# Performance work log

Measured on AMD Instinct MI355X. Metric: run time of the kernel, lower is better.

Reference implementation:

```python
import jax, jax.numpy as jnp
import numpy as np
from math import sqrt

NUM_HEAD = 16
HEAD_DIM = 64  # out_dim // num_head = 1024 // 16


def setup_inputs() -> dict:
    key = jax.random.key(0)
    ks = jax.random.split(key, 6)
    B, L, D = 2, 2048, 1024
    s = 1.0 / sqrt(D)
    return {
        "x": jax.random.normal(ks[0], (B, L, D), jnp.float32),
        "position_embedding": jax.random.normal(ks[1], (1, NUM_HEAD, L, L), jnp.float32),
        "Wq": jax.random.normal(ks[2], (D, D), jnp.float32) * s,
        "Wk": jax.random.normal(ks[3], (D, D), jnp.float32) * s,
        "Wv": jax.random.normal(ks[4], (D, D), jnp.float32) * s,
        "Wo": jax.random.normal(ks[5], (D, D), jnp.float32) * s,
    }


def reference(x, position_embedding, Wq, Wk, Wv, Wo):
    # x: [B, L, D]; torch Linear(y = x @ W.T) -> here weights stored as [in, out]
    B, L, D = x.shape
    H, Hd = NUM_HEAD, HEAD_DIM
    q = (x @ Wq).reshape(B, L, H, Hd).transpose(0, 2, 1, 3)  # [B,H,L,Hd]
    k = (x @ Wk).reshape(B, L, H, Hd).transpose(0, 2, 1, 3)
    v = (x @ Wv).reshape(B, L, H, Hd).transpose(0, 2, 1, 3)
    scores = jnp.einsum("bhqd,bhkd->bhqk", q, k) / sqrt(Hd)  # [B,H,L,L]
    scores = scores + position_embedding
    attn = jax.nn.softmax(scores, axis=-1)
    out = jnp.einsum("bhqk,bhkd->bhqd", attn, v)  # [B,H,L,Hd]
    out = out.transpose(0, 2, 1, 3).reshape(B, L, H * Hd)
    return out @ Wo
```

## Files before the change

kernel.cpp:

```cpp
#include <hip/hip_runtime.h>
#include <hip/hip_bf16.h>
#include <stdint.h>

typedef __hip_bfloat16 bf16;
typedef __attribute__((ext_vector_type(8))) short bf16x8;
typedef __attribute__((ext_vector_type(4))) float f32x4;
typedef __attribute__((ext_vector_type(16))) float f32x16;
typedef __attribute__((ext_vector_type(4))) unsigned u32x4;

#define B_  2
#define L_  2048
#define D_  1024
#define H_  16
#define HD_ 64
#define BH_ 32
#define L2E 1.4426950408889634f

#define DEV static __device__ __forceinline__

DEV short f2bf(float f) {
    bf16 h = __float2bfloat16(f);
    return __builtin_bit_cast(short, h);
}

DEV unsigned pk2(float lo, float hi) {
    unsigned a = (unsigned short)__builtin_bit_cast(unsigned short, __float2bfloat16(lo));
    unsigned b = (unsigned short)__builtin_bit_cast(unsigned short, __float2bfloat16(hi));
    return a | (b << 16);
}

DEV f32x4 mfma16(bf16x8 a, bf16x8 b, f32x4 c) {
    return __builtin_amdgcn_mfma_f32_16x16x32_bf16(a, b, c, 0, 0, 0);
}
DEV f32x16 mfma32(bf16x8 a, bf16x8 b, f32x16 c) {
    return __builtin_amdgcn_mfma_f32_32x32x16_bf16(a, b, c, 0, 0, 0);
}

DEV void async_ld16(const void* g, void* lds_uniform) {
    __builtin_amdgcn_global_load_lds((const __attribute__((address_space(1))) void*)g,
                                     (__attribute__((address_space(3))) void*)lds_uniform,
                                     16, 0, 0);
}

DEV int swz(int row, int col) {
    int blk = (row << 3) + (col >> 3);
    blk ^= (row & 7);
    return (blk << 3) + (col & 7);
}

__global__ __launch_bounds__(256) void k_cast_x(const float* __restrict__ x,
                                                bf16* __restrict__ xb, int n8) {
    int i = blockIdx.x * 256 + threadIdx.x;
    if (i >= n8) return;
    const float4* src = (const float4*)x + (size_t)i * 2;
    float4 a = src[0], b = src[1];
    bf16x8 v;
    v[0]=f2bf(a.x); v[1]=f2bf(a.y); v[2]=f2bf(a.z); v[3]=f2bf(a.w);
    v[4]=f2bf(b.x); v[5]=f2bf(b.y); v[6]=f2bf(b.z); v[7]=f2bf(b.w);
    *(bf16x8*)(xb + (size_t)i * 8) = v;
}

__global__ __launch_bounds__(256) void k_cast_wT(const float* __restrict__ W0, const float* __restrict__ W1,
                                                 const float* __restrict__ W2, const float* __restrict__ W3,
                                                 bf16* __restrict__ WT) {
    const float* W = (blockIdx.z == 0) ? W0 : (blockIdx.z == 1) ? W1 : (blockIdx.z == 2) ? W2 : W3;
    __shared__ float tile[64][65];
    const int r0 = blockIdx.y * 64, c0 = blockIdx.x * 64;
    const int tx = threadIdx.x & 63, ty = threadIdx.x >> 6;
    #pragma unroll
    for (int i = 0; i < 16; ++i) {
        int r = ty + i * 4;
        tile[r][tx] = W[(size_t)(r0 + r) * D_ + c0 + tx];
    }
    __syncthreads();
    bf16* out = WT + (size_t)blockIdx.z * D_ * D_;
    #pragma unroll
    for (int i = 0; i < 16; ++i) {
        int n = ty + i * 4;
        out[(size_t)(c0 + n) * D_ + r0 + tx] = __float2bfloat16(tile[tx][n]);
    }
}

template <int MODE>
__global__ __launch_bounds__(256) void k_gemm(const bf16* __restrict__ A, const bf16* __restrict__ BT,
                                              void* __restrict__ C) {
    __shared__ __align__(16) bf16 As[128 * 64];
    __shared__ __align__(16) bf16 Bs[128 * 64];
    const int t = threadIdx.x;
    const int w = t >> 6, lane = t & 63;
    const int lr = lane & 15, lg = lane >> 4;
    const int wr = (w >> 1) * 64, wc = (w & 1) * 64;
    const size_t am0 = (size_t)blockIdx.y * 128;
    const size_t bn0 = (size_t)blockIdx.x * 128;

    f32x4 acc[4][4] = {};

    for (int kt = 0; kt < 1024 / 64; ++kt) {
        const int k0 = kt * 64;
        if (kt) __syncthreads();
        #pragma unroll
        for (int c = 0; c < 4; ++c) {
            int phys = c * 256 + t;
            int lb = phys ^ ((phys >> 3) & 7);
            int row = lb >> 3, cb = lb & 7;
            int ldsoff = (c * 256 + w * 64) * 8;
            async_ld16(A  + (am0 + row) * 1024 + k0 + cb * 8, (void*)(As + ldsoff));
            async_ld16(BT + (bn0 + row) * 1024 + k0 + cb * 8, (void*)(Bs + ldsoff));
        }
        __syncthreads();
        bf16x8 af[4][2], bfv[4][2];
        #pragma unroll
        for (int mi = 0; mi < 4; ++mi)
            #pragma unroll
            for (int ks = 0; ks < 2; ++ks)
                af[mi][ks] = *(const bf16x8*)(As + swz(wr + mi * 16 + lr, ks * 32 + lg * 8));
        #pragma unroll
        for (int ni = 0; ni < 4; ++ni)
            #pragma unroll
            for (int ks = 0; ks < 2; ++ks)
                bfv[ni][ks] = *(const bf16x8*)(Bs + swz(wc + ni * 16 + lr, ks * 32 + lg * 8));
        #pragma unroll
        for (int mi = 0; mi < 4; ++mi)
            #pragma unroll
            for (int ni = 0; ni < 4; ++ni) {
                acc[mi][ni] = mfma16(af[mi][0], bfv[ni][0], acc[mi][ni]);
                acc[mi][ni] = mfma16(af[mi][1], bfv[ni][1], acc[mi][ni]);
            }
    }

    #pragma unroll
    for (int mi = 0; mi < 4; ++mi)
        #pragma unroll
        for (int ni = 0; ni < 4; ++ni)
            #pragma unroll
            for (int j = 0; j < 4; ++j) {
                size_t gm = am0 + wr + mi * 16 + lg * 4 + j;
                size_t gn = bn0 + wc + ni * 16 + lr;
                float v = acc[mi][ni][j];
                if (MODE == 0) {
                    int which = (int)(gn >> 10);
                    int h = (int)((gn >> 6) & 15);
                    int d = (int)(gn & 63);
                    int bb = (int)(gm >> 11);
                    int l = (int)(gm & 2047);
                    if (which == 0) v *= 0.18033688011112042f;
                    bf16* dst = (bf16*)C + (size_t)which * ((size_t)BH_ * L_ * HD_);
                    dst[((size_t)(bb * H_ + h) * L_ + l) * HD_ + d] = __float2bfloat16(v);
                } else {
                    ((float*)C)[gm * 1024 + gn] = v;
                }
            }
}

__global__ __launch_bounds__(256) void k_transpose_v(const bf16* __restrict__ Vb, bf16* __restrict__ VTb) {
    __shared__ __align__(16) short tile[64][80];
    const int bh = blockIdx.y;
    const int l0 = blockIdx.x * 64;
    const int t = threadIdx.x;
    const int rr = t >> 2, cc = (t & 3) * 16;
    const short* src = (const short*)(Vb + ((size_t)bh * L_ + l0 + rr) * HD_ + cc);
    *(bf16x8*)&tile[rr][cc]     = *(const bf16x8*)src;
    *(bf16x8*)&tile[rr][cc + 8] = *(const bf16x8*)(src + 8);
    __syncthreads();
    bf16x8 v0, v1;
    #pragma unroll
    for (int i = 0; i < 8; ++i) v0[i] = tile[cc + i][rr];
    #pragma unroll
    for (int i = 0; i < 8; ++i) v1[i] = tile[cc + 8 + i][rr];
    short* dst = (short*)(VTb + ((size_t)bh * HD_ + rr) * L_ + l0 + cc);
    *(bf16x8*)dst       = v0;
    *(bf16x8*)(dst + 8) = v1;
}

__global__ __launch_bounds__(256, 3) void k_attn(const bf16* __restrict__ Qb, const bf16* __restrict__ Kb,
                                                 const bf16* __restrict__ VTb, const float* __restrict__ PE,
                                                 bf16* __restrict__ Ob) {
    __shared__ __align__(16) char shm[49152];

    const int bid = blockIdx.x;
    const int sw  = (bid & 7) * 64 + (bid >> 3);
    const int qt  = sw & 31, h = sw >> 5;
    const int t   = threadIdx.x;
    const int w   = t >> 6, l = t & 63;
    const int qs  = w & 1, b = w >> 1;
    const int q0  = qt * 64 + qs * 32;
    const int lq  = l & 31;
    const int lh  = l >> 5;

    const int pb = (lq >> 2) & 3;
    const int prow = lq + (pb == 1 ? 4 : (pb == 2 ? -4 : 0));

    bf16x8 Qf[4];
    #pragma unroll
    for (int dm = 0; dm < 4; ++dm)
        Qf[dm] = *(const bf16x8*)(Qb + ((size_t)(b * H_ + h) * L_ + q0 + lq) * HD_ + dm * 16 + lh * 8);

    const bf16*  kb  = Kb  + (size_t)(b * H_ + h) * L_ * HD_;
    const bf16*  vbp = VTb + (size_t)(b * H_ + h) * HD_ * L_;
    const float* peq = PE  + ((size_t)h * L_ + q0) * L_;

    const int k_srcoff  = (l >> 3) * HD_ + (((l & 7) ^ (l >> 3)) * 8);
    const int v_srcoff  = (l >> 2) * L_  + (((l & 3) ^ ((l >> 2) & 3)) * 8);
    const int pe_srcoff = (l >> 3) * L_  + (((l & 7) ^ (l >> 3)) * 4);

    int kro[4];
    #pragma unroll
    for (int dm = 0; dm < 4; ++dm)
        kro[dm] = prow * 64 + (((dm * 2 + lh) ^ (prow & 7)) * 8);
    int vro[2][2];
    #pragma unroll
    for (int d0 = 0; d0 < 2; ++d0)
        #pragma unroll
        for (int m = 0; m < 2; ++m)
            vro[d0][m] = (d0 * 32 + lq) * 32 + (((m * 2 + lh) ^ (lq & 3)) * 8);
    int peo[4];
    #pragma unroll
    for (int g = 0; g < 4; ++g)
        peo[g] = lq * 32 + ((((g >> 1) * 4 + (g & 1) + lh * 2) ^ (lq & 7)) * 4);

#define SH_K(BUF)  (shm + (BUF) * 24576 + b * 4096)
#define SH_V(BUF)  (shm + (BUF) * 24576 + 8192 + b * 4096)
#define SH_PE(BUF) (shm + (BUF) * 24576 + 16384 + qs * 4096)

    f32x16 o[2] = {};
    float mrun = -3e38f, lpart = 0.f;

#define STAGE(BUF, TILE) {                                                              \
    const int kv0_ = (TILE) * 32;                                                       \
    _Pragma("unroll") for (int i = 0; i < 2; ++i) {                                     \
        const int c = 2 * qs + i;                                                       \
        async_ld16(kb + (size_t)(kv0_ + c * 8) * HD_ + k_srcoff, (void*)(SH_K(BUF) + c * 1024)); \
    }                                                                                   \
    _Pragma("unroll") for (int i = 0; i < 2; ++i) {                                     \
        const int c = 2 * qs + i;                                                       \
        async_ld16(vbp + (size_t)(c * 16) * L_ + kv0_ + v_srcoff, (void*)(SH_V(BUF) + c * 1024)); \
    }                                                                                   \
    _Pragma("unroll") for (int i = 0; i < 2; ++i) {                                     \
        const int c = 2 * b + i;                                                        \
        async_ld16(peq + (size_t)(c * 8) * L_ + kv0_ + pe_srcoff, (void*)(SH_PE(BUF) + c * 1024)); \
    }                                                                                   \
}

#define COMPUTE(BUF) {                                                                  \
    const bf16*  KL = (const bf16*)SH_K(BUF);                                           \
    const bf16*  VL = (const bf16*)SH_V(BUF);                                           \
    const float* PL = (const float*)SH_PE(BUF);                                         \
    bf16x8 kf0_ = *(const bf16x8*)(KL + kro[0]);                                        \
    bf16x8 kf1_ = *(const bf16x8*)(KL + kro[1]);                                        \
    bf16x8 kf2_ = *(const bf16x8*)(KL + kro[2]);                                        \
    bf16x8 kf3_ = *(const bf16x8*)(KL + kro[3]);                                        \
    f32x16 s = {};                                                                      \
    s = mfma32(kf0_, Qf[0], s);                                                         \
    s = mfma32(kf1_, Qf[1], s);                                                         \
    s = mfma32(kf2_, Qf[2], s);                                                         \
    s = mfma32(kf3_, Qf[3], s);                                                         \
    float4 pef_[4];                                                                     \
    _Pragma("unroll") for (int g = 0; g < 4; ++g)                                       \
        pef_[g] = *(const float4*)(PL + peo[g]);                                        \
    float v_[16];                                                                       \
    _Pragma("unroll") for (int r = 0; r < 16; ++r)                                      \
        v_[r] = fmaf(pef_[r >> 2][r & 3], L2E, s[r]);                                   \
    float t0_ = fmaxf(fmaxf(v_[0], v_[1]), fmaxf(v_[2], v_[3]));                        \
    float t1_ = fmaxf(fmaxf(v_[4], v_[5]), fmaxf(v_[6], v_[7]));                        \
    float t2_ = fmaxf(fmaxf(v_[8], v_[9]), fmaxf(v_[10], v_[11]));                      \
    float t3_ = fmaxf(fmaxf(v_[12], v_[13]), fmaxf(v_[14], v_[15]));                    \
    float vmh_ = fmaxf(fmaxf(t0_, t1_), fmaxf(t2_, t3_));                               \
    float vm_ = fmaxf(vmh_, __shfl_xor(vmh_, 32, 64));                                  \
    float mold_ = mrun;                                                                 \
    float mnew_ = mold_;                                                                \
    if (!__all(vm_ <= mold_ + 10.f)) {                                                  \
        mnew_ = fmaxf(mold_, vm_);                                                      \
        float scl_ = __builtin_amdgcn_exp2f(mold_ - mnew_);                             \
        mrun = mnew_;                                                                   \
        lpart *= scl_;                                                                  \
        _Pragma("unroll") for (int r = 0; r < 16; ++r) { o[0][r] *= scl_; o[1][r] *= scl_; } \
    }                                                                                   \
    float p_[16], ssum_ = 0.f;                                                          \
    _Pragma("unroll") for (int r = 0; r < 16; ++r) {                                    \
        p_[r] = __builtin_amdgcn_exp2f(v_[r] - mnew_);                                  \
        ssum_ += p_[r];                                                                 \
    }                                                                                   \
    lpart += ssum_;                                                                     \
    unsigned a_[8];                                                                     \
    _Pragma("unroll") for (int j = 0; j < 8; ++j)                                       \
        a_[j] = pk2(p_[2 * j], p_[2 * j + 1]);                                          \
    u32x4 w0v_ = { a_[0], a_[1], a_[2], a_[3] };                                        \
    u32x4 w1v_ = { a_[4], a_[5], a_[6], a_[7] };                                        \
    bf16x8 pf0_ = __builtin_bit_cast(bf16x8, w0v_);                                     \
    bf16x8 pf1_ = __builtin_bit_cast(bf16x8, w1v_);                                     \
    o[0] = mfma32(*(const bf16x8*)(VL + vro[0][0]), pf0_, o[0]);                        \
    o[0] = mfma32(*(const bf16x8*)(VL + vro[0][1]), pf1_, o[0]);                        \
    o[1] = mfma32(*(const bf16x8*)(VL + vro[1][0]), pf0_, o[1]);                        \
    o[1] = mfma32(*(const bf16x8*)(VL + vro[1][1]), pf1_, o[1]);                        \
}

    STAGE(0, 0)
    STAGE(1, 1)
    asm volatile("s_waitcnt vmcnt(6)" ::: "memory");
    __builtin_amdgcn_s_barrier();

    for (int tt = 0; tt < 64; ++tt) {
        const int buf = tt & 1;
        if (buf == 0) { COMPUTE(0) } else { COMPUTE(1) }
        __builtin_amdgcn_s_barrier();
        const int pft = (tt + 2 < 64) ? tt + 2 : 63;
        if (buf == 0) { STAGE(0, pft) } else { STAGE(1, pft) }
        asm volatile("s_waitcnt vmcnt(6)" ::: "memory");
        __builtin_amdgcn_s_barrier();
    }
#undef COMPUTE
#undef STAGE
#undef SH_K
#undef SH_V
#undef SH_PE

    asm volatile("s_waitcnt vmcnt(0)" ::: "memory");

    float lsum = lpart + __shfl_xor(lpart, 32, 64);
    float inv = __builtin_amdgcn_rcpf(lsum);
    #pragma unroll
    for (int d0 = 0; d0 < 2; ++d0)
        #pragma unroll
        for (int r = 0; r < 16; r += 2) {
            float e0 = o[d0][r] * inv;
            float e1 = o[d0][r + 1] * inv;
            int d = d0 * 32 + ((r & 3) + 8 * (r >> 2)) + lh * 4;
            *(unsigned*)(Ob + ((size_t)b * L_ + q0 + lq) * D_ + h * HD_ + d) = pk2(e0, e1);
        }
}

extern "C" void kernel_launch(void* const* d_in, const int* in_sizes, int n_in,
                              void* d_out, int out_size, void* d_ws, size_t ws_size,
                              hipStream_t stream) {
    const float* x  = (const float*)d_in[0];
    const float* pe = (const float*)d_in[1];
    const float* Wq = (const float*)d_in[2];
    const float* Wk = (const float*)d_in[3];
    const float* Wv = (const float*)d_in[4];
    const float* Wo = (const float*)d_in[5];
    float* out = (float*)d_out;

    const size_t MD = (size_t)4096 * 1024;
    const size_t HS = (size_t)BH_ * L_ * HD_;

    bf16* Xb  = (bf16*)d_ws;
    bf16* WT  = Xb + MD;
    bf16* Qb  = WT + MD;
    bf16* Kb  = Qb + HS;
    bf16* Vb  = Kb + HS;
    bf16* VTb = Vb + HS;
    bf16* Ob  = VTb + HS;

    k_cast_x<<<2048, 256, 0, stream>>>(x, Xb, 4096 * 1024 / 8);
    k_cast_wT<<<dim3(16, 16, 4), 256, 0, stream>>>(Wq, Wk, Wv, Wo, WT);
    k_gemm<0><<<dim3(24, 32), 256, 0, stream>>>(Xb, WT, (void*)Qb);
    k_transpose_v<<<dim3(32, 32), 256, 0, stream>>>(Vb, VTb);
    k_attn<<<512, 256, 0, stream>>>(Qb, Kb, VTb, pe, Ob);
    k_gemm<1><<<dim3(8, 32), 256, 0, stream>>>(Ob, WT + (size_t)3072 * 1024, (void*)out);
}
```

Before: 172.9 us.

## Load position bias directly to registers and share V tile across batch waves

Position-embedding values are now loaded straight from global memory into registers, two tiles ahead, instead of being staged through LDS. V staging is rewritten so the four waves cooperatively load a shared 64-wide V tile covering both batches with a new swizzle, and the loop is unrolled by two so buffer indices are static. LDS use drops from 48KB to 32KB per block, which may allow more resident blocks, but PE register prefetch raises register pressure and the waitcnt accounting changes.

```diff
diff --git a/kernel.cpp b/kernel.cpp
--- a/kernel.cpp
+++ b/kernel.cpp
@@ -175,7 +175,7 @@
 __global__ __launch_bounds__(256, 3) void k_attn(const bf16* __restrict__ Qb, const bf16* __restrict__ Kb,
                                                  const bf16* __restrict__ VTb, const float* __restrict__ PE,
                                                  bf16* __restrict__ Ob) {
-    __shared__ __align__(16) char shm[49152];
+    __shared__ __align__(16) char shm[32768];
 
     const int bid = blockIdx.x;
     const int sw  = (bid & 7) * 64 + (bid >> 3);
@@ -195,13 +195,18 @@
     for (int dm = 0; dm < 4; ++dm)
         Qf[dm] = *(const bf16x8*)(Qb + ((size_t)(b * H_ + h) * L_ + q0 + lq) * HD_ + dm * 16 + lh * 8);
 
-    const bf16*  kb  = Kb  + (size_t)(b * H_ + h) * L_ * HD_;
-    const bf16*  vbp = VTb + (size_t)(b * H_ + h) * HD_ * L_;
-    const float* peq = PE  + ((size_t)h * L_ + q0) * L_;
-
-    const int k_srcoff  = (l >> 3) * HD_ + (((l & 7) ^ (l >> 3)) * 8);
-    const int v_srcoff  = (l >> 2) * L_  + (((l & 3) ^ ((l >> 2) & 3)) * 8);
-    const int pe_srcoff = (l >> 3) * L_  + (((l & 7) ^ (l >> 3)) * 4);
+    const bf16*  kb    = Kb  + (size_t)(b * H_ + h) * L_ * HD_;
+    const bf16*  vbase = VTb + (size_t)h * HD_ * L_;
+    const float* perow = PE  + ((size_t)h * L_ + q0 + lq) * L_;
+
+    const int k_srcoff = (l >> 3) * HD_ + (((l & 7) ^ (l >> 3)) * 8);
+    const int vlb   = (l & 7) ^ (l >> 3);
+    const size_t v_lane = (size_t)(vlb >> 2) * ((size_t)H_ * HD_ * L_)
+                        + (size_t)(l >> 3) * L_ + (vlb & 3) * 8;
+    int peoff[4];
+    #pragma unroll
+    for (int g = 0; g < 4; ++g)
+        peoff[g] = (g >> 1) * 16 + (g & 1) * 4 + lh * 8;
 
     int kro[4];
     #pragma unroll
@@ -212,18 +217,14 @@
     for (int d0 = 0; d0 < 2; ++d0)
         #pragma unroll
         for (int m = 0; m < 2; ++m)
-            vro[d0][m] = (d0 * 32 + lq) * 32 + (((m * 2 + lh) ^ (lq & 3)) * 8);
-    int peo[4];
-    #pragma unroll
-    for (int g = 0; g < 4; ++g)
-        peo[g] = lq * 32 + ((((g >> 1) * 4 + (g & 1) + lh * 2) ^ (lq & 7)) * 4);
-
-#define SH_K(BUF)  (shm + (BUF) * 24576 + b * 4096)
-#define SH_V(BUF)  (shm + (BUF) * 24576 + 8192 + b * 4096)
-#define SH_PE(BUF) (shm + (BUF) * 24576 + 16384 + qs * 4096)
+            vro[d0][m] = (d0 * 32 + lq) * 64 + (((b * 4 + m * 2 + lh) ^ (lq & 7)) * 8);
+
+#define SH_K(BUF) (shm + (BUF) * 16384 + b * 4096)
+#define SH_V(BUF) (shm + (BUF) * 16384 + 8192)
 
     f32x16 o[2] = {};
     float mrun = -3e38f, lpart = 0.f;
+    float4 pe0[4], pe1[4];
 
 #define STAGE(BUF, TILE) {                                                              \
     const int kv0_ = (TILE) * 32;                                                       \
@@ -232,19 +233,19 @@
         async_ld16(kb + (size_t)(kv0_ + c * 8) * HD_ + k_srcoff, (void*)(SH_K(BUF) + c * 1024)); \
     }                                                                                   \
     _Pragma("unroll") for (int i = 0; i < 2; ++i) {                                     \
-        const int c = 2 * qs + i;                                                       \
-        async_ld16(vbp + (size_t)(c * 16) * L_ + kv0_ + v_srcoff, (void*)(SH_V(BUF) + c * 1024)); \
+        const int cv = 2 * w + i;                                                       \
+        async_ld16(vbase + v_lane + (size_t)(cv * 8) * L_ + kv0_, (void*)(SH_V(BUF) + cv * 1024)); \
     }                                                                                   \
-    _Pragma("unroll") for (int i = 0; i < 2; ++i) {                                     \
-        const int c = 2 * b + i;                                                        \
-        async_ld16(peq + (size_t)(c * 8) * L_ + kv0_ + pe_srcoff, (void*)(SH_PE(BUF) + c * 1024)); \
-    }                                                                                   \
-}
-
-#define COMPUTE(BUF) {                                                                  \
-    const bf16*  KL = (const bf16*)SH_K(BUF);                                           \
-    const bf16*  VL = (const bf16*)SH_V(BUF);                                           \
-    const float* PL = (const float*)SH_PE(BUF);                                         \
+}
+
+#define PELOAD(DST, TILE) {                                                             \
+    _Pragma("unroll") for (int g = 0; g < 4; ++g)                                       \
+        DST[g] = *(const float4*)(perow + (size_t)(TILE) * 32 + peoff[g]);              \
+}
+
+#define COMPUTE(BUF, PEA) {                                                             \
+    const bf16* KL = (const bf16*)SH_K(BUF);                                            \
+    const bf16* VL = (const bf16*)SH_V(BUF);                                            \
     bf16x8 kf0_ = *(const bf16x8*)(KL + kro[0]);                                        \
     bf16x8 kf1_ = *(const bf16x8*)(KL + kro[1]);                                        \
     bf16x8 kf2_ = *(const bf16x8*)(KL + kro[2]);                                        \
@@ -254,12 +255,9 @@
     s = mfma32(kf1_, Qf[1], s);                                                         \
     s = mfma32(kf2_, Qf[2], s);                                                         \
     s = mfma32(kf3_, Qf[3], s);                                                         \
-    float4 pef_[4];                                                                     \
-    _Pragma("unroll") for (int g = 0; g < 4; ++g)                                       \
-        pef_[g] = *(const float4*)(PL + peo[g]);                                        \
     float v_[16];                                                                       \
     _Pragma("unroll") for (int r = 0; r < 16; ++r)                                      \
-        v_[r] = fmaf(pef_[r >> 2][r & 3], L2E, s[r]);                                   \
+        v_[r] = fmaf(PEA[r >> 2][r & 3], L2E, s[r]);                                    \
     float t0_ = fmaxf(fmaxf(v_[0], v_[1]), fmaxf(v_[2], v_[3]));                        \
     float t1_ = fmaxf(fmaxf(v_[4], v_[5]), fmaxf(v_[6], v_[7]));                        \
     float t2_ = fmaxf(fmaxf(v_[8], v_[9]), fmaxf(v_[10], v_[11]));                      \
@@ -295,24 +293,34 @@
 }
 
     STAGE(0, 0)
+    PELOAD(pe0, 0)
     STAGE(1, 1)
-    asm volatile("s_waitcnt vmcnt(6)" ::: "memory");
+    PELOAD(pe1, 1)
+    asm volatile("s_waitcnt vmcnt(8)" ::: "memory");
     __builtin_amdgcn_s_barrier();
 
-    for (int tt = 0; tt < 64; ++tt) {
-        const int buf = tt & 1;
-        if (buf == 0) { COMPUTE(0) } else { COMPUTE(1) }
+    for (int tp = 0; tp < 32; ++tp) {
+        const int e = 2 * tp;
+        const int pfA = (e + 2 < 64) ? e + 2 : 63;
+        const int pfB = (e + 3 < 64) ? e + 3 : 63;
+        COMPUTE(0, pe0)
         __builtin_amdgcn_s_barrier();
-        const int pft = (tt + 2 < 64) ? tt + 2 : 63;
-        if (buf == 0) { STAGE(0, pft) } else { STAGE(1, pft) }
-        asm volatile("s_waitcnt vmcnt(6)" ::: "memory");
+        STAGE(0, pfA)
+        PELOAD(pe0, pfA)
+        asm volatile("s_waitcnt vmcnt(8)" ::: "memory");
+        __builtin_amdgcn_s_barrier();
+        COMPUTE(1, pe1)
+        __builtin_amdgcn_s_barrier();
+        STAGE(1, pfB)
+        PELOAD(pe1, pfB)
+        asm volatile("s_waitcnt vmcnt(8)" ::: "memory");
         __builtin_amdgcn_s_barrier();
     }
 #undef COMPUTE
+#undef PELOAD
 #undef STAGE
 #undef SH_K
 #undef SH_V
-#undef SH_PE
 
     asm volatile("s_waitcnt vmcnt(0)" ::: "memory");
 
```

Measured after the change: 199.9 us. 15.6% more time.

## Triple-buffer attention K/V/PE staging and share V tile across batch warps

Applied to the files above, without the earlier changes.

Deepens the async global-to-LDS pipeline from two to three buffers, prefetching three tiles ahead with a wait that lets 12 loads stay in flight. The V tile layout is changed so that both batch halves are loaded into one shared 64-wide swizzled LDS region, with each warp loading a slice. LDS grows to 72KB, and launch bounds drop from 3 to 2 blocks per CU, trading occupancy for more latency hiding.

```diff
diff --git a/kernel.cpp b/kernel.cpp
--- a/kernel.cpp
+++ b/kernel.cpp
@@ -172,10 +172,10 @@
     *(bf16x8*)(dst + 8) = v1;
 }
 
-__global__ __launch_bounds__(256, 3) void k_attn(const bf16* __restrict__ Qb, const bf16* __restrict__ Kb,
+__global__ __launch_bounds__(256, 2) void k_attn(const bf16* __restrict__ Qb, const bf16* __restrict__ Kb,
                                                  const bf16* __restrict__ VTb, const float* __restrict__ PE,
                                                  bf16* __restrict__ Ob) {
-    __shared__ __align__(16) char shm[49152];
+    __shared__ __align__(16) char shm[73728];
 
     const int bid = blockIdx.x;
     const int sw  = (bid & 7) * 64 + (bid >> 3);
@@ -195,13 +195,15 @@
     for (int dm = 0; dm < 4; ++dm)
         Qf[dm] = *(const bf16x8*)(Qb + ((size_t)(b * H_ + h) * L_ + q0 + lq) * HD_ + dm * 16 + lh * 8);
 
-    const bf16*  kb  = Kb  + (size_t)(b * H_ + h) * L_ * HD_;
-    const bf16*  vbp = VTb + (size_t)(b * H_ + h) * HD_ * L_;
-    const float* peq = PE  + ((size_t)h * L_ + q0) * L_;
+    const bf16*  kb    = Kb  + (size_t)(b * H_ + h) * L_ * HD_;
+    const bf16*  vbase = VTb + (size_t)h * HD_ * L_;
+    const float* peq   = PE  + ((size_t)h * L_ + q0) * L_;
 
     const int k_srcoff  = (l >> 3) * HD_ + (((l & 7) ^ (l >> 3)) * 8);
-    const int v_srcoff  = (l >> 2) * L_  + (((l & 3) ^ ((l >> 2) & 3)) * 8);
-    const int pe_srcoff = (l >> 3) * L_  + (((l & 7) ^ (l >> 3)) * 4);
+    const int vlb = (l & 7) ^ (l >> 3);
+    const size_t v_lane = (size_t)(vlb >> 2) * ((size_t)H_ * HD_ * L_)
+                        + (size_t)(l >> 3) * L_ + (vlb & 3) * 8;
+    const int pe_srcoff = (l >> 3) * L_ + (((l & 7) ^ (l >> 3)) * 4);
 
     int kro[4];
     #pragma unroll
@@ -212,14 +214,14 @@
     for (int d0 = 0; d0 < 2; ++d0)
         #pragma unroll
         for (int m = 0; m < 2; ++m)
-            vro[d0][m] = (d0 * 32 + lq) * 32 + (((m * 2 + lh) ^ (lq & 3)) * 8);
+            vro[d0][m] = (d0 * 32 + lq) * 64 + (((b * 4 + m * 2 + lh) ^ (lq & 7)) * 8);
     int peo[4];
     #pragma unroll
     for (int g = 0; g < 4; ++g)
         peo[g] = lq * 32 + ((((g >> 1) * 4 + (g & 1) + lh * 2) ^ (lq & 7)) * 4);
 
 #define SH_K(BUF)  (shm + (BUF) * 24576 + b * 4096)
-#define SH_V(BUF)  (shm + (BUF) * 24576 + 8192 + b * 4096)
+#define SH_V(BUF)  (shm + (BUF) * 24576 + 8192)
 #define SH_PE(BUF) (shm + (BUF) * 24576 + 16384 + qs * 4096)
 
     f32x16 o[2] = {};
@@ -232,8 +234,8 @@
         async_ld16(kb + (size_t)(kv0_ + c * 8) * HD_ + k_srcoff, (void*)(SH_K(BUF) + c * 1024)); \
     }                                                                                   \
     _Pragma("unroll") for (int i = 0; i < 2; ++i) {                                     \
-        const int c = 2 * qs + i;                                                       \
-        async_ld16(vbp + (size_t)(c * 16) * L_ + kv0_ + v_srcoff, (void*)(SH_V(BUF) + c * 1024)); \
+        const int cv = 2 * w + i;                                                       \
+        async_ld16(vbase + v_lane + (size_t)(cv * 8) * L_ + kv0_, (void*)(SH_V(BUF) + cv * 1024)); \
     }                                                                                   \
     _Pragma("unroll") for (int i = 0; i < 2; ++i) {                                     \
         const int c = 2 * b + i;                                                        \
@@ -294,20 +296,31 @@
     o[1] = mfma32(*(const bf16x8*)(VL + vro[1][1]), pf1_, o[1]);                        \
 }
 
+#define STEP(BUF, T, PFT) {                                                             \
+    asm volatile("s_waitcnt vmcnt(12)" ::: "memory");        \
+    __builtin_amdgcn_s_barrier();                         \
+    COMPUTE(BUF)                                                                        \
+    __builtin_amdgcn_s_barrier();                             \
+    STAGE(BUF, PFT)                                                                     \
+}
+
     STAGE(0, 0)
     STAGE(1, 1)
-    asm volatile("s_waitcnt vmcnt(6)" ::: "memory");
+    STAGE(2, 2)
+
+    for (int tp = 0; tp < 21; ++tp) {
+        const int e = 3 * tp;
+        const int f0 = (e + 3 < 64) ? e + 3 : 63;
+        const int f1 = (e + 4 < 64) ? e + 4 : 63;
+        const int f2 = (e + 5 < 64) ? e + 5 : 63;
+        STEP(0, e,     f0)
+        STEP(1, e + 1, f1)
+        STEP(2, e + 2, f2)
+    }
+    asm volatile("s_waitcnt vmcnt(12)" ::: "memory");
     __builtin_amdgcn_s_barrier();
-
-    for (int tt = 0; tt < 64; ++tt) {
-        const int buf = tt & 1;
-        if (buf == 0) { COMPUTE(0) } else { COMPUTE(1) }
-        __builtin_amdgcn_s_barrier();
-        const int pft = (tt + 2 < 64) ? tt + 2 : 63;
-        if (buf == 0) { STAGE(0, pft) } else { STAGE(1, pft) }
-        asm volatile("s_waitcnt vmcnt(6)" ::: "memory");
-        __builtin_amdgcn_s_barrier();
-    }
+    COMPUTE(0)
+#undef STEP
 #undef COMPUTE
 #undef STAGE
 #undef SH_K
```

After: 166.7 us. 1.04x faster.
